# Kernel optimization log

Measured on AMD Instinct MI355X. Metric: run time of the kernel, lower is better.

## Reference

```python
import jax, jax.numpy as jnp
import numpy as np

VOCAB = 32000
HIDDEN = 512


def setup_inputs() -> dict:
    key = jax.random.key(0)
    k1, k2, k3, k4 = jax.random.split(key, 4)
    B, L = 64, 2048  # batch of trees, leaves per (complete binary) tree
    leaf_ids = jax.random.randint(k1, (B, L), 0, VOCAB)
    emb = jax.random.normal(k2, (VOCAB, HIDDEN), dtype=jnp.float32)
    # nn.Linear(2H, H): weight [H, 2H], bias [H]
    lim = 1.0 / np.sqrt(2 * HIDDEN)
    W = jax.random.uniform(k3, (HIDDEN, 2 * HIDDEN), minval=-lim, maxval=lim, dtype=jnp.float32)
    b = jax.random.uniform(k4, (HIDDEN,), minval=-lim, maxval=lim, dtype=jnp.float32)
    return {"leaf_ids": leaf_ids, "emb": emb, "W": W, "b": b}


def reference(leaf_ids, emb, W, b):
    # Preterminal nodes: embed leaf token then activation (matches original order).
    h = jnp.tanh(emb[leaf_ids])  # [B, L, H]
    B, L, H = h.shape
    n_levels = int(np.log2(L))
    # Bottom-up: each internal node concatenates its two children -> linear -> tanh.
    # All same-depth nodes processed as one batched GEMM.
    for _ in range(n_levels):
        n = h.shape[1]
        pairs = h.reshape(B, n // 2, 2 * H)          # concat(left, right) along feature dim
        h = jnp.tanh(jnp.einsum('bnf,hf->bnh', pairs, W) + b)
    return h  # [B, 1, H] root hidden state per tree
```

## Files before the change

### kernel.cpp

```cpp
#include <hip/hip_runtime.h>
#include <stdint.h>

typedef __attribute__((ext_vector_type(8))) short short8;
typedef __attribute__((ext_vector_type(4))) float floatx4;

__device__ __forceinline__ unsigned short f2bf(float x) {
    unsigned int u = __builtin_bit_cast(unsigned int, x);
    unsigned int r = (u + 0x7FFFu + ((u >> 16) & 1u)) >> 16;
    return (unsigned short)r;
}
__device__ __forceinline__ float bf2f(unsigned short x) {
    unsigned int u = ((unsigned int)x) << 16;
    return __builtin_bit_cast(float, u);
}

__device__ __forceinline__ float fast_tanh(float x) {
    float xc = fminf(fmaxf(x, -10.0f), 10.0f);
    float e  = __expf(2.0f * xc);
    float d  = e + 1.0f;
    float r  = __builtin_amdgcn_rcpf(d);
    r = r * (2.0f - d * r);
    return (e - 1.0f) * r;
}

__global__ void wconv(const float4* __restrict__ W4, ushort4* __restrict__ Wb4) {
    int i = blockIdx.x * 256 + threadIdx.x;
    float4 v = W4[i];
    ushort4 o;
    o.x = f2bf(v.x); o.y = f2bf(v.y); o.z = f2bf(v.z); o.w = f2bf(v.w);
    Wb4[i] = o;
}

__global__ void tconv(const float4* __restrict__ emb4, ushort4* __restrict__ embT4) {
    int i = blockIdx.x * 256 + threadIdx.x;
    float4 v = emb4[i];
    ushort4 o;
    o.x = f2bf(fast_tanh(v.x)); o.y = f2bf(fast_tanh(v.y));
    o.z = f2bf(fast_tanh(v.z)); o.w = f2bf(fast_tanh(v.w));
    embT4[i] = o;
}

__global__ void lvl1_add(const int* __restrict__ ids, const ushort* __restrict__ PQ,
                         const float* __restrict__ bias, ushort* __restrict__ h1)
{
    int idx = blockIdx.x * 256 + threadIdx.x;
    int m = idx >> 6;
    int c = (idx & 63) << 3;
    const int il = ids[2 * m], ir = ids[2 * m + 1];
    const short8 p = *reinterpret_cast<const short8*>(PQ + (size_t)il * 512 + c);
    const short8 q = *reinterpret_cast<const short8*>(PQ + 16384000 + (size_t)ir * 512 + c);
    const float4 b0 = *reinterpret_cast<const float4*>(bias + c);
    const float4 b1 = *reinterpret_cast<const float4*>(bias + c + 4);
    short8 o;
    o[0] = (short)f2bf(fast_tanh(bf2f((unsigned short)p[0]) + bf2f((unsigned short)q[0]) + b0.x));
    o[1] = (short)f2bf(fast_tanh(bf2f((unsigned short)p[1]) + bf2f((unsigned short)q[1]) + b0.y));
    o[2] = (short)f2bf(fast_tanh(bf2f((unsigned short)p[2]) + bf2f((unsigned short)q[2]) + b0.z));
    o[3] = (short)f2bf(fast_tanh(bf2f((unsigned short)p[3]) + bf2f((unsigned short)q[3]) + b0.w));
    o[4] = (short)f2bf(fast_tanh(bf2f((unsigned short)p[4]) + bf2f((unsigned short)q[4]) + b1.x));
    o[5] = (short)f2bf(fast_tanh(bf2f((unsigned short)p[5]) + bf2f((unsigned short)q[5]) + b1.y));
    o[6] = (short)f2bf(fast_tanh(bf2f((unsigned short)p[6]) + bf2f((unsigned short)q[6]) + b1.z));
    o[7] = (short)f2bf(fast_tanh(bf2f((unsigned short)p[7]) + bf2f((unsigned short)q[7]) + b1.w));
    *reinterpret_cast<short8*>(h1 + (size_t)idx * 8) = o;
}

#define STG264(buf, k0)                                                         \
    do {                                                                        \
        _Pragma("unroll")                                                       \
        for (int p = 0; p < 4; ++p) {                                           \
            __builtin_amdgcn_global_load_lds(                                   \
                (const __attribute__((address_space(1))) void*)(Ap + (size_t)p * 64 * ASTR + (k0)), \
                (__attribute__((address_space(3))) void*)&sA[buf][p * 4096 + tid * 8], 16, 0, 0); \
            __builtin_amdgcn_global_load_lds(                                   \
                (const __attribute__((address_space(1))) void*)(Bp + (size_t)p * 64 * 1024 + (k0)), \
                (__attribute__((address_space(3))) void*)&sB[buf][p * 4096 + tid * 8], 16, 0, 0); \
        }                                                                       \
    } while (0)

#define CMP264(buf)                                                             \
    do {                                                                        \
        _Pragma("unroll")                                                       \
        for (int ks = 0; ks < 2; ++ks) {                                        \
            const int kq_ = ks * 4 + lh;                                        \
            const int sw_ = ((kq_ ^ (l15 & 7)) << 3);                           \
            short8 a_[8], b_[4];                                                \
            _Pragma("unroll")                                                   \
            for (int ni = 0; ni < 4; ++ni)                                      \
                b_[ni] = *reinterpret_cast<const short8*>(&sB[buf][(rB + ni * 16) * 64 + sw_]); \
            _Pragma("unroll")                                                   \
            for (int mi = 0; mi < 8; ++mi)                                      \
                a_[mi] = *reinterpret_cast<const short8*>(&sA[buf][(rA + mi * 16) * 64 + sw_]); \
            __builtin_amdgcn_s_setprio(1);                                      \
            _Pragma("unroll")                                                   \
            for (int mi = 0; mi < 8; ++mi)                                      \
                _Pragma("unroll")                                               \
                for (int ni = 0; ni < 4; ++ni)                                  \
                    acc[mi][ni] = __builtin_amdgcn_mfma_f32_16x16x32_bf16(      \
                        a_[mi], b_[ni], acc[mi][ni], 0, 0, 0);                  \
            __builtin_amdgcn_s_setprio(0);                                      \
        }                                                                       \
    } while (0)

template<int ASTR, int NT, int MODE>
__global__ __launch_bounds__(512)
void gemm256(const ushort* __restrict__ A, const ushort* __restrict__ Bt,
             const float* __restrict__ bias, ushort* __restrict__ outb)
{
    __shared__ alignas(16) ushort sA[2][16384];
    __shared__ alignas(16) ushort sB[2][16384];

    const int tid  = threadIdx.x;
    const int lane = tid & 63;
    const int w    = tid >> 6;
    const int wr   = w >> 2, wc = w & 3;
    const int l15  = lane & 15;
    const int lh   = lane >> 4;

    int mt, ntile, koff = 0;
    size_t obase = 0;
    if constexpr (MODE == 0) {
        const int nb  = gridDim.x;
        const int per = nb >> 3;
        const int lin = (blockIdx.x & 7) * per + (blockIdx.x >> 3);
        mt = lin >> 1; ntile = lin & 1;
    } else {
        const int bid = blockIdx.x;
        int g, sel;
        if (bid < 480) { g = (bid >> 5) * 8 + (bid & 7); sel = (bid >> 3) & 3; }
        else           { g = 120 + ((bid - 480) >> 2);   sel = (bid - 480) & 3; }
        const int table = sel >> 1;
        mt = g; ntile = sel & 1;
        koff  = table << 9;
        obase = (size_t)table * 16384000;
    }
    const int m0 = mt * 256, n0 = ntile * 256;

    const int r0 = tid >> 3;
    const int s0 = tid & 7;
    const int swz = ((s0 ^ (r0 & 7)) << 3);
    const ushort* Ap = A  + (size_t)(m0 + r0) * ASTR + swz;
    const ushort* Bp = Bt + (size_t)(n0 + r0) * 1024 + koff + swz;

    const int rA = wr * 128 + l15;
    const int rB = wc * 64  + l15;

    floatx4 acc[8][4] = {};

    STG264(0, 0);
    for (int t = 0; t + 2 < NT; t += 2) {
        asm volatile("s_barrier" ::: "memory");
        STG264(1, (t + 1) * 64);
        asm volatile("s_waitcnt vmcnt(8)" ::: "memory");
        CMP264(0);
        asm volatile("s_barrier" ::: "memory");
        STG264(0, (t + 2) * 64);
        asm volatile("s_waitcnt vmcnt(8)" ::: "memory");
        CMP264(1);
    }
    asm volatile("s_barrier" ::: "memory");
    STG264(1, (NT - 1) * 64);
    asm volatile("s_waitcnt vmcnt(8)" ::: "memory");
    CMP264(0);
    asm volatile("s_barrier" ::: "memory");
    asm volatile("s_waitcnt vmcnt(0)" ::: "memory");
    CMP264(1);

    const int mrow = lh * 4;
    #pragma unroll
    for (int mi = 0; mi < 8; ++mi) {
        #pragma unroll
        for (int ni = 0; ni < 4; ++ni) {
            const int n = n0 + wc * 64 + ni * 16 + l15;
            #pragma unroll
            for (int j = 0; j < 4; ++j) {
                const int m = m0 + wr * 128 + mi * 16 + mrow + j;
                if constexpr (MODE == 0) {
                    float v = fast_tanh(acc[mi][ni][j] + bias[n]);
                    outb[(size_t)m * 512 + n] = f2bf(v);
                } else {
                    outb[obase + (size_t)m * 512 + n] = f2bf(acc[mi][ni][j]);
                }
            }
        }
    }
}

#define STAGE_(buf, k0)                                                         \
    do {                                                                        \
        __builtin_amdgcn_global_load_lds(                                       \
            (const __attribute__((address_space(1))) void*)(Ap + (k0)),         \
            (__attribute__((address_space(3))) void*)&sA[buf][tid * 8], 16, 0, 0); \
        __builtin_amdgcn_global_load_lds(                                       \
            (const __attribute__((address_space(1))) void*)(Ap + 64 * 1024 + (k0)), \
            (__attribute__((address_space(3))) void*)&sA[buf][2048 + tid * 8], 16, 0, 0); \
        __builtin_amdgcn_global_load_lds(                                       \
            (const __attribute__((address_space(1))) void*)(Bp + (k0)),         \
            (__attribute__((address_space(3))) void*)&sB[buf][tid * 8], 16, 0, 0); \
        __builtin_amdgcn_global_load_lds(                                       \
            (const __attribute__((address_space(1))) void*)(Bp + 64 * 1024 + (k0)), \
            (__attribute__((address_space(3))) void*)&sB[buf][2048 + tid * 8], 16, 0, 0); \
    } while (0)

#define COMPUTE_(cur)                                                           \
    do {                                                                        \
        short8 a_[4], b_[4];                                                    \
        _Pragma("unroll")                                                       \
        for (int mi = 0; mi < 4; ++mi)                                          \
            a_[mi] = *reinterpret_cast<const short8*>(&sA[cur][(rA + mi * 16) * 32 + kksw]); \
        _Pragma("unroll")                                                       \
        for (int ni = 0; ni < 4; ++ni)                                          \
            b_[ni] = *reinterpret_cast<const short8*>(&sB[cur][(rB + ni * 16) * 32 + kksw]); \
        __builtin_amdgcn_s_setprio(1);                                          \
        _Pragma("unroll")                                                       \
        for (int mi = 0; mi < 4; ++mi)                                          \
            _Pragma("unroll")                                                   \
            for (int ni = 0; ni < 4; ++ni)                                      \
                acc[mi][ni] = __builtin_amdgcn_mfma_f32_16x16x32_bf16(          \
                    a_[mi], b_[ni], acc[mi][ni], 0, 0, 0);                      \
        __builtin_amdgcn_s_setprio(0);                                          \
    } while (0)

__global__ __launch_bounds__(256)
void level_gemm(const ushort* __restrict__ A, const ushort* __restrict__ Bt,
                const float* __restrict__ bias,
                ushort* __restrict__ outb, int M)
{
    const int nb  = gridDim.x;
    int bid = blockIdx.x;
    const int per = nb >> 3;
    const int lin = (bid & 7) * per + (bid >> 3);
    const int mt = lin >> 2, nt = lin & 3;
    const int m0 = mt * 128, n0 = nt * 128;

    __shared__ alignas(16) ushort sA[3][4096];
    __shared__ alignas(16) ushort sB[3][4096];

    const int tid  = threadIdx.x;
    const int lane = tid & 63;
    const int w    = tid >> 6;
    const int wr   = w >> 1, wc = w & 1;

    const int sr    = tid >> 2;
    const int swcol = (((tid & 3) ^ ((tid >> 3) & 3)) << 3);
    const ushort* Ap = A  + (size_t)(m0 + sr) * 1024 + swcol;
    const ushort* Bp = Bt + (size_t)(n0 + sr) * 1024 + swcol;

    const int rA   = wr * 64 + (lane & 15);
    const int rB   = wc * 64 + (lane & 15);
    const int kksw = (((lane >> 4) ^ ((lane >> 1) & 3)) << 3);

    floatx4 acc[4][4] = {};

    STAGE_(0, 0);
    STAGE_(1, 32);
    for (int t = 0; t < 30; t += 3) {
        asm volatile("s_barrier" ::: "memory");
        STAGE_(2, (t + 2) * 32);
        asm volatile("s_waitcnt vmcnt(4)" ::: "memory");
        COMPUTE_(0);
        asm volatile("s_barrier" ::: "memory");
        STAGE_(0, (t + 3) * 32);
        asm volatile("s_waitcnt vmcnt(4)" ::: "memory");
        COMPUTE_(1);
        asm volatile("s_barrier" ::: "memory");
        STAGE_(1, (t + 4) * 32);
        asm volatile("s_waitcnt vmcnt(4)" ::: "memory");
        COMPUTE_(2);
    }
    asm volatile("s_barrier" ::: "memory");
    asm volatile("s_waitcnt vmcnt(0)" ::: "memory");
    COMPUTE_(0);
    asm volatile("s_barrier" ::: "memory");
    asm volatile("s_waitcnt vmcnt(0)" ::: "memory");
    COMPUTE_(1);

    const int mrow = (lane >> 4) * 4;
    const int ncol = lane & 15;
    #pragma unroll
    for (int mi = 0; mi < 4; ++mi)
        #pragma unroll
        for (int ni = 0; ni < 4; ++ni) {
            const int n = n0 + wc * 64 + ni * 16 + ncol;
            const float bb = bias[n];
            #pragma unroll
            for (int j = 0; j < 4; ++j) {
                const int m = m0 + wr * 64 + mi * 16 + mrow + j;
                float v = fast_tanh(acc[mi][ni][j] + bb);
                outb[(size_t)m * 512 + n] = f2bf(v);
            }
        }
}

__global__ __launch_bounds__(256)
void small_gemm(const ushort* __restrict__ A, const ushort* __restrict__ Bt,
                const float* __restrict__ bias,
                ushort* __restrict__ outb, float* __restrict__ outf, int last)
{
    __shared__ alignas(16) ushort sA[3][4096];
    __shared__ alignas(16) ushort sB[3][4096];

    const int tid  = threadIdx.x;
    const int lane = tid & 63;
    const int w    = tid >> 6;
    const int l15  = lane & 15;
    const int lh   = lane >> 4;
    const int mt   = blockIdx.x >> 3, nt = blockIdx.x & 7;
    const int m0   = mt * 64, n0 = nt * 64;

    const int r0 = tid >> 3;
    const int s0 = tid & 7;
    const int swz = ((s0 ^ (r0 & 7)) << 3);
    const ushort* Ap = A  + (size_t)(m0 + r0) * 1024 + swz;
    const ushort* Bp = Bt + (size_t)(n0 + r0) * 1024 + swz;

#define STG6(buf, k0)                                                           \
    do {                                                                        \
        __builtin_amdgcn_global_load_lds(                                       \
            (const __attribute__((address_space(1))) void*)(Ap + (k0)),         \
            (__attribute__((address_space(3))) void*)&sA[buf][tid * 8], 16, 0, 0); \
        __builtin_amdgcn_global_load_lds(                                       \
            (const __attribute__((address_space(1))) void*)(Ap + 32 * 1024 + (k0)), \
            (__attribute__((address_space(3))) void*)&sA[buf][2048 + tid * 8], 16, 0, 0); \
        __builtin_amdgcn_global_load_lds(                                       \
            (const __attribute__((address_space(1))) void*)(Bp + (k0)),         \
            (__attribute__((address_space(3))) void*)&sB[buf][tid * 8], 16, 0, 0); \
        __builtin_amdgcn_global_load_lds(                                       \
            (const __attribute__((address_space(1))) void*)(Bp + 32 * 1024 + (k0)), \
            (__attribute__((address_space(3))) void*)&sB[buf][2048 + tid * 8], 16, 0, 0); \
    } while (0)

    const int rb = w * 16 + l15;
    floatx4 acc[4] = {};

#define CMP6(buf)                                                               \
    do {                                                                        \
        _Pragma("unroll")                                                       \
        for (int ks = 0; ks < 2; ++ks) {                                        \
            const int kq = ks * 4 + lh;                                         \
            const short8 b_ = *reinterpret_cast<const short8*>(                 \
                &sB[buf][rb * 64 + ((kq ^ (rb & 7)) << 3)]);                    \
            __builtin_amdgcn_s_setprio(1);                                      \
            _Pragma("unroll")                                                   \
            for (int mi = 0; mi < 4; ++mi) {                                    \
                const int ra = mi * 16 + l15;                                   \
                const short8 a_ = *reinterpret_cast<const short8*>(             \
                    &sA[buf][ra * 64 + ((kq ^ (l15 & 7)) << 3)]);               \
                acc[mi] = __builtin_amdgcn_mfma_f32_16x16x32_bf16(              \
                    a_, b_, acc[mi], 0, 0, 0);                                  \
            }                                                                   \
            __builtin_amdgcn_s_setprio(0);                                      \
        }                                                                       \
    } while (0)

    STG6(0, 0);
    STG6(1, 64);
    for (int t3 = 0; t3 < 12; t3 += 3) {
        asm volatile("s_barrier" ::: "memory");
        STG6(2, (t3 + 2) * 64);
        asm volatile("s_waitcnt vmcnt(4)" ::: "memory");
        CMP6(0);
        asm volatile("s_barrier" ::: "memory");
        STG6(0, (t3 + 3) * 64);
        asm volatile("s_waitcnt vmcnt(4)" ::: "memory");
        CMP6(1);
        asm volatile("s_barrier" ::: "memory");
        STG6(1, (t3 + 4) * 64);
        asm volatile("s_waitcnt vmcnt(4)" ::: "memory");
        CMP6(2);
    }
    asm volatile("s_barrier" ::: "memory");
    STG6(2, 14 * 64);
    asm volatile("s_waitcnt vmcnt(8)" ::: "memory");
    CMP6(0);
    asm volatile("s_barrier" ::: "memory");
    STG6(0, 15 * 64);
    asm volatile("s_waitcnt vmcnt(8)" ::: "memory");
    CMP6(1);
    asm volatile("s_barrier" ::: "memory");
    asm volatile("s_waitcnt vmcnt(4)" ::: "memory");
    CMP6(2);
    asm volatile("s_barrier" ::: "memory");
    asm volatile("s_waitcnt vmcnt(0)" ::: "memory");
    CMP6(0);
#undef CMP6
#undef STG6

    const int n  = n0 + w * 16 + l15;
    const float bb = bias[n];
    #pragma unroll
    for (int mi = 0; mi < 4; ++mi) {
        #pragma unroll
        for (int j = 0; j < 4; ++j) {
            const int m = m0 + mi * 16 + lh * 4 + j;
            float v = fast_tanh(acc[mi][j] + bb);
            if (last) outf[(size_t)m * 512 + n] = v;
            else      outb[(size_t)m * 512 + n] = f2bf(v);
        }
    }
}

extern "C" void kernel_launch(void* const* d_in, const int* in_sizes, int n_in,
                              void* d_out, int out_size, void* d_ws, size_t ws_size,
                              hipStream_t stream) {
    const int*   ids  = (const int*)d_in[0];
    const float* emb  = (const float*)d_in[1];
    const float* W    = (const float*)d_in[2];
    const float* bias = (const float*)d_in[3];
    float* out = (float*)d_out;

    unsigned short* Wb   = (unsigned short*)d_ws;
    unsigned short* embT = Wb + 524288;
    unsigned short* PQ   = embT + 16384000;
    unsigned short* hB   = PQ + 32768000;
    unsigned short* hA   = hB + 33554432;

    wconv<<<512, 256, 0, stream>>>((const float4*)W, (ushort4*)Wb);
    tconv<<<16000, 256, 0, stream>>>((const float4*)emb, (ushort4*)embT);

    gemm256<512, 8, 1><<<500, 512, 0, stream>>>(embT, Wb, bias, PQ);
    lvl1_add<<<16384, 256, 0, stream>>>(ids, PQ, bias, hB);

    gemm256<1024, 16, 0><<<256, 512, 0, stream>>>(hB, Wb, bias, hA);

    level_gemm<<<512, 256, 0, stream>>>(hA, Wb, bias, hB, 16384);
    level_gemm<<<256, 256, 0, stream>>>(hB, Wb, bias, hA, 8192);

    int M = 4096;
    for (int l = 5; l <= 11; ++l) {
        const unsigned short* in = (l & 1) ? hA : hB;
        unsigned short*       ob = (l & 1) ? hB : hA;
        small_gemm<<<(M / 64) * 8, 256, 0, stream>>>(in, Wb, bias, ob, out,
                                                     l == 11 ? 1 : 0);
        M >>= 1;
    }
}
```

Baseline: 256.1 us.

## Split gemm256 K-tiles into half-stages with finer-grained load/compute pipelining

The 256x256 GEMM kernel now stages each 64-wide K tile as two 32-wide halves with a new 4-column XOR swizzle. It issues the next half-stage load before waiting and computing the current one. The intent is finer overlap of global-to-LDS traffic with MFMA work and shorter stalls per barrier. The cost is twice as many barriers per K tile, and the ordering now puts the wait before the barrier, which changes how the loads in flight are tracked. The other kernels only get their waitcnt and barrier asm wrapped in macros, with the same ordering.

```diff
diff --git a/kernel.cpp b/kernel.cpp
--- a/kernel.cpp
+++ b/kernel.cpp
@@ -63,42 +63,46 @@
     *reinterpret_cast<short8*>(h1 + (size_t)idx * 8) = o;
 }
 
-#define STG264(buf, k0)                                                         \
-    do {                                                                        \
-        _Pragma("unroll")                                                       \
-        for (int p = 0; p < 4; ++p) {                                           \
-            __builtin_amdgcn_global_load_lds(                                   \
-                (const __attribute__((address_space(1))) void*)(Ap + (size_t)p * 64 * ASTR + (k0)), \
-                (__attribute__((address_space(3))) void*)&sA[buf][p * 4096 + tid * 8], 16, 0, 0); \
-            __builtin_amdgcn_global_load_lds(                                   \
-                (const __attribute__((address_space(1))) void*)(Bp + (size_t)p * 64 * 1024 + (k0)), \
-                (__attribute__((address_space(3))) void*)&sB[buf][p * 4096 + tid * 8], 16, 0, 0); \
-        }                                                                       \
-    } while (0)
-
-#define CMP264(buf)                                                             \
-    do {                                                                        \
-        _Pragma("unroll")                                                       \
-        for (int ks = 0; ks < 2; ++ks) {                                        \
-            const int kq_ = ks * 4 + lh;                                        \
-            const int sw_ = ((kq_ ^ (l15 & 7)) << 3);                           \
-            short8 a_[8], b_[4];                                                \
+#define S4(buf, h, t)                                                           \
+    do {                                                                        \
+        const int kb_ = (t) * 64 + (h) * 32;                                    \
+        __builtin_amdgcn_global_load_lds(                                       \
+            (const __attribute__((address_space(1))) void*)(ApS + kb_),         \
+            (__attribute__((address_space(3))) void*)&sA[buf][(h) * 8192 + tid * 8], 16, 0, 0); \
+        __builtin_amdgcn_global_load_lds(                                       \
+            (const __attribute__((address_space(1))) void*)(ApS + (size_t)128 * ASTR + kb_), \
+            (__attribute__((address_space(3))) void*)&sA[buf][(h) * 8192 + 4096 + tid * 8], 16, 0, 0); \
+        __builtin_amdgcn_global_load_lds(                                       \
+            (const __attribute__((address_space(1))) void*)(BpS + kb_),         \
+            (__attribute__((address_space(3))) void*)&sB[buf][(h) * 8192 + tid * 8], 16, 0, 0); \
+        __builtin_amdgcn_global_load_lds(                                       \
+            (const __attribute__((address_space(1))) void*)(BpS + 128 * 1024 + kb_), \
+            (__attribute__((address_space(3))) void*)&sB[buf][(h) * 8192 + 4096 + tid * 8], 16, 0, 0); \
+    } while (0)
+
+#define C4(buf, ks)                                                             \
+    do {                                                                        \
+        short8 a_[8], b_[4];                                                    \
+        _Pragma("unroll")                                                       \
+        for (int ni = 0; ni < 4; ++ni)                                          \
+            b_[ni] = *reinterpret_cast<const short8*>(                          \
+                &sB[buf][(ks) * 8192 + (rB + ni * 16) * 32 + kx]);              \
+        _Pragma("unroll")                                                       \
+        for (int mi = 0; mi < 8; ++mi)                                          \
+            a_[mi] = *reinterpret_cast<const short8*>(                          \
+                &sA[buf][(ks) * 8192 + (rA + mi * 16) * 32 + kx]);              \
+        __builtin_amdgcn_s_setprio(1);                                          \
+        _Pragma("unroll")                                                       \
+        for (int mi = 0; mi < 8; ++mi)                                          \
             _Pragma("unroll")                                                   \
             for (int ni = 0; ni < 4; ++ni)                                      \
-                b_[ni] = *reinterpret_cast<const short8*>(&sB[buf][(rB + ni * 16) * 64 + sw_]); \
-            _Pragma("unroll")                                                   \
-            for (int mi = 0; mi < 8; ++mi)                                      \
-                a_[mi] = *reinterpret_cast<const short8*>(&sA[buf][(rA + mi * 16) * 64 + sw_]); \
-            __builtin_amdgcn_s_setprio(1);                                      \
-            _Pragma("unroll")                                                   \
-            for (int mi = 0; mi < 8; ++mi)                                      \
-                _Pragma("unroll")                                               \
-                for (int ni = 0; ni < 4; ++ni)                                  \
-                    acc[mi][ni] = __builtin_amdgcn_mfma_f32_16x16x32_bf16(      \
-                        a_[mi], b_[ni], acc[mi][ni], 0, 0, 0);                  \
-            __builtin_amdgcn_s_setprio(0);                                      \
-        }                                                                       \
-    } while (0)
+                acc[mi][ni] = __builtin_amdgcn_mfma_f32_16x16x32_bf16(          \
+                    a_[mi], b_[ni], acc[mi][ni], 0, 0, 0);                      \
+        __builtin_amdgcn_s_setprio(0);                                          \
+    } while (0)
+
+#define VMC(n) asm volatile("s_waitcnt vmcnt(" #n ")" ::: "memory")
+#define BAR()  asm volatile("s_barrier" ::: "memory")
 
 template<int ASTR, int NT, int MODE>
 __global__ __launch_bounds__(512)
@@ -134,35 +138,31 @@
     }
     const int m0 = mt * 256, n0 = ntile * 256;
 
-    const int r0 = tid >> 3;
-    const int s0 = tid & 7;
-    const int swz = ((s0 ^ (r0 & 7)) << 3);
-    const ushort* Ap = A  + (size_t)(m0 + r0) * ASTR + swz;
-    const ushort* Bp = Bt + (size_t)(n0 + r0) * 1024 + koff + swz;
+    const int r  = tid >> 2;
+    const int sl = tid & 3;
+    const int xsl8 = ((sl ^ ((r >> 1) & 3)) << 3);
+    const ushort* ApS = A  + (size_t)(m0 + r) * ASTR + xsl8;
+    const ushort* BpS = Bt + (size_t)(n0 + r) * 1024 + koff + xsl8;
 
     const int rA = wr * 128 + l15;
     const int rB = wc * 64  + l15;
+    const int kx = ((lh ^ ((l15 >> 1) & 3)) << 3);
 
     floatx4 acc[8][4] = {};
 
-    STG264(0, 0);
-    for (int t = 0; t + 2 < NT; t += 2) {
-        asm volatile("s_barrier" ::: "memory");
-        STG264(1, (t + 1) * 64);
-        asm volatile("s_waitcnt vmcnt(8)" ::: "memory");
-        CMP264(0);
-        asm volatile("s_barrier" ::: "memory");
-        STG264(0, (t + 2) * 64);
-        asm volatile("s_waitcnt vmcnt(8)" ::: "memory");
-        CMP264(1);
-    }
-    asm volatile("s_barrier" ::: "memory");
-    STG264(1, (NT - 1) * 64);
-    asm volatile("s_waitcnt vmcnt(8)" ::: "memory");
-    CMP264(0);
-    asm volatile("s_barrier" ::: "memory");
-    asm volatile("s_waitcnt vmcnt(0)" ::: "memory");
-    CMP264(1);
+    S4(0, 0, 0);
+    S4(0, 1, 0);
+
+    for (int t = 0; t < NT - 2; t += 2) {
+        S4(1, 0, t + 1); VMC(8); BAR(); C4(0, 0);
+        S4(1, 1, t + 1); VMC(8); BAR(); C4(0, 1);
+        S4(0, 0, t + 2); VMC(8); BAR(); C4(1, 0);
+        S4(0, 1, t + 2); VMC(8); BAR(); C4(1, 1);
+    }
+    S4(1, 0, NT - 1); VMC(8); BAR(); C4(0, 0);
+    S4(1, 1, NT - 1); VMC(8); BAR(); C4(0, 1);
+    VMC(4); BAR(); C4(1, 0);
+    VMC(0); BAR(); C4(1, 1);
 
     const int mrow = lh * 4;
     #pragma unroll
@@ -253,25 +253,12 @@
     STAGE_(0, 0);
     STAGE_(1, 32);
     for (int t = 0; t < 30; t += 3) {
-        asm volatile("s_barrier" ::: "memory");
-        STAGE_(2, (t + 2) * 32);
-        asm volatile("s_waitcnt vmcnt(4)" ::: "memory");
-        COMPUTE_(0);
-        asm volatile("s_barrier" ::: "memory");
-        STAGE_(0, (t + 3) * 32);
-        asm volatile("s_waitcnt vmcnt(4)" ::: "memory");
-        COMPUTE_(1);
-        asm volatile("s_barrier" ::: "memory");
-        STAGE_(1, (t + 4) * 32);
-        asm volatile("s_waitcnt vmcnt(4)" ::: "memory");
-        COMPUTE_(2);
-    }
-    asm volatile("s_barrier" ::: "memory");
-    asm volatile("s_waitcnt vmcnt(0)" ::: "memory");
-    COMPUTE_(0);
-    asm volatile("s_barrier" ::: "memory");
-    asm volatile("s_waitcnt vmcnt(0)" ::: "memory");
-    COMPUTE_(1);
+        BAR(); STAGE_(2, (t + 2) * 32); VMC(4); COMPUTE_(0);
+        BAR(); STAGE_(0, (t + 3) * 32); VMC(4); COMPUTE_(1);
+        BAR(); STAGE_(1, (t + 4) * 32); VMC(4); COMPUTE_(2);
+    }
+    BAR(); VMC(0); COMPUTE_(0);
+    BAR(); VMC(0); COMPUTE_(1);
 
     const int mrow = (lane >> 4) * 4;
     const int ncol = lane & 15;
@@ -354,33 +341,14 @@
     STG6(0, 0);
     STG6(1, 64);
     for (int t3 = 0; t3 < 12; t3 += 3) {
-        asm volatile("s_barrier" ::: "memory");
-        STG6(2, (t3 + 2) * 64);
-        asm volatile("s_waitcnt vmcnt(4)" ::: "memory");
-        CMP6(0);
-        asm volatile("s_barrier" ::: "memory");
-        STG6(0, (t3 + 3) * 64);
-        asm volatile("s_waitcnt vmcnt(4)" ::: "memory");
-        CMP6(1);
-        asm volatile("s_barrier" ::: "memory");
-        STG6(1, (t3 + 4) * 64);
-        asm volatile("s_waitcnt vmcnt(4)" ::: "memory");
-        CMP6(2);
-    }
-    asm volatile("s_barrier" ::: "memory");
-    STG6(2, 14 * 64);
-    asm volatile("s_waitcnt vmcnt(8)" ::: "memory");
-    CMP6(0);
-    asm volatile("s_barrier" ::: "memory");
-    STG6(0, 15 * 64);
-    asm volatile("s_waitcnt vmcnt(8)" ::: "memory");
-    CMP6(1);
-    asm volatile("s_barrier" ::: "memory");
-    asm volatile("s_waitcnt vmcnt(4)" ::: "memory");
-    CMP6(2);
-    asm volatile("s_barrier" ::: "memory");
-    asm volatile("s_waitcnt vmcnt(0)" ::: "memory");
-    CMP6(0);
+        BAR(); STG6(2, (t3 + 2) * 64); VMC(4); CMP6(0);
+        BAR(); STG6(0, (t3 + 3) * 64); VMC(4); CMP6(1);
+        BAR(); STG6(1, (t3 + 4) * 64); VMC(4); CMP6(2);
+    }
+    BAR(); STG6(2, 14 * 64); VMC(8); CMP6(0);
+    BAR(); STG6(0, 15 * 64); VMC(8); CMP6(1);
+    BAR(); VMC(4); CMP6(2);
+    BAR(); VMC(0); CMP6(0);
 #undef CMP6
 #undef STG6
 
```

Result: no change. 258.9 us (+1.1%).
